# Optimization experiments

Measured on AMD Instinct MI355X. Metric: run time of the kernel, lower is better.

## Reference

```python
import jax, jax.numpy as jnp
import numpy as np

N_NODES = 50000
N_EDGES = 800000
NC = 16
FDIM = 13
FHID = 64


def setup_inputs() -> dict:
    key = jax.random.key(0)
    ks = jax.random.split(key, 10)
    inp = {
        "hx": jax.random.normal(ks[0], (N_NODES, NC), jnp.float32),
        "edgefeats": jax.random.normal(ks[1], (N_EDGES, FDIM), jnp.float32),
        "idxn": jax.random.randint(ks[2], (N_EDGES,), 0, N_NODES, jnp.int32),
        "edge_dst": jnp.sort(jax.random.randint(ks[3], (N_EDGES,), 0, N_NODES, jnp.int32)),
        "fnet_w1": jax.random.normal(ks[4], (FDIM, FHID), jnp.float32) * 0.3,
        "fnet_b1": jnp.zeros((FHID,), jnp.float32),
        "fnet_w2": jax.random.normal(ks[5], (FHID, NC * NC), jnp.float32) * 0.05,
        "fnet_b2": jnp.zeros((NC * NC,), jnp.float32),
        "w_ih": jax.random.normal(ks[6], (3 * NC, NC), jnp.float32) * 0.25,
        "w_hh": jax.random.normal(ks[7], (3 * NC, NC), jnp.float32) * 0.25,
        "b_ih": jnp.zeros((3 * NC,), jnp.float32),
        "b_hh": jnp.zeros((3 * NC,), jnp.float32),
    }
    return inp


def _gru_cell(x, h, w_ih, w_hh, b_ih, b_hh):
    gi = x @ w_ih.T + b_ih  # [N, 3*nc]
    gh = h @ w_hh.T + b_hh
    i_r, i_z, i_n = jnp.split(gi, 3, axis=1)
    h_r, h_z, h_n = jnp.split(gh, 3, axis=1)
    r = jax.nn.sigmoid(i_r + h_r)
    z = jax.nn.sigmoid(i_z + h_z)
    n = jnp.tanh(i_n + r * h_n)
    return (1.0 - z) * n + z * h


def reference(hx, edgefeats, idxn, edge_dst, fnet_w1, fnet_b1, fnet_w2, fnet_b2,
              w_ih, w_hh, b_ih, b_hh):
    n_nodes, nc = hx.shape
    # Filter-generating network: per-edge [nc, nc] weight matrices (shared over iterations).
    w_flat = jax.nn.relu(edgefeats @ fnet_w1 + fnet_b1) @ fnet_w2 + fnet_b2
    W = w_flat.reshape(-1, nc, nc)  # [E, nc, nc]
    # Degree normalization per destination node.
    deg = jax.ops.segment_sum(jnp.ones_like(edge_dst, dtype=hx.dtype), edge_dst,
                              num_segments=n_nodes)
    inv_deg = (1.0 / jnp.maximum(deg, 1.0))[:, None]  # [N, 1]

    def gconv(h):
        msgs = jnp.einsum('ec,ecd->ed', h[idxn], W)  # gather + per-edge matmul
        agg = jax.ops.segment_sum(msgs, edge_dst, num_segments=n_nodes)
        return agg * inv_deg

    def cell(inp, h):
        return _gru_cell(inp, h, w_ih, w_hh, b_ih, b_hh)

    hxs = [hx]
    h1 = cell(gconv(hx), hx); hxs.append(h1)
    h2 = cell(gconv(h1), h1); hxs.append(h2)
    h3 = cell(gconv(h2), h2)
    s1 = h1 + h3; hxs.append(s1)
    h4 = cell(gconv(s1), s1); hxs.append(h4)
    h5 = cell(gconv(h4), h4)
    s2 = h3 + h5; hxs.append(s2)
    h6 = cell(gconv(s2), s2); hxs.append(h6)
    h7 = cell(gconv(h6), h6)
    s3 = h5 + h7; hxs.append(s3)
    h8 = cell(gconv(s3), s3); hxs.append(h8)
    h9 = cell(gconv(h8), h8)
    s4 = h7 + h9; hxs.append(s4)
    h10 = cell(gconv(s4), s4); hxs.append(h10)
    return jnp.concatenate(hxs, axis=1)  # cat_all=True -> [N, 11*nc]
```

## Files before the change

### kernel.cpp

```cpp
#include <hip/hip_runtime.h>

#define NN 50000
#define NE 800000
#define OUTC 176

typedef unsigned int uint32;
typedef short bf16x8 __attribute__((ext_vector_type(8)));
typedef float f32x4 __attribute__((ext_vector_type(4)));

__device__ __forceinline__ uint32 f2bf_rne(float f) {
  union { float f; uint32 u; } v; v.f = f;
  uint32 u = v.u;
  return (u + 0x7FFFu + ((u >> 16) & 1u)) >> 16;
}
__device__ __forceinline__ uint32 packbf2(float a, float b) {
  return f2bf_rne(a) | (f2bf_rne(b) << 16);
}
__device__ __forceinline__ float blo(uint32 u) {
  union { uint32 x; float f; } t; t.x = u << 16; return t.f;
}
__device__ __forceinline__ float bhi(uint32 u) {
  union { uint32 x; float f; } t; t.x = u & 0xFFFF0000u; return t.f;
}
__device__ __forceinline__ float bf2f(unsigned short v) {
  union { uint32 x; float f; } t; t.x = ((uint32)v) << 16; return t.f;
}
__device__ __forceinline__ float sb2f(uint32 w, int b) {
  return (float)((int)(w << (24 - 8 * b)) >> 24);
}

__global__ __launch_bounds__(256) void deg_count_kernel(const int* __restrict__ edst,
                                                        float* __restrict__ deg) {
  int e = blockIdx.x * 256 + threadIdx.x;
  if (e < NE) atomicAdd(&deg[edst[e]], 1.0f);
}

__global__ __launch_bounds__(256) void deg_inv_kernel(float* __restrict__ deg) {
  int n = blockIdx.x * 256 + threadIdx.x;
  if (n < NN) deg[n] = 1.0f / fmaxf(deg[n], 1.0f);
}

__global__ __launch_bounds__(256) void copy_col0_kernel(const float* __restrict__ hx,
                                                        float* __restrict__ out) {
  int n = blockIdx.x * 256 + threadIdx.x;
  if (n >= NN) return;
  const float4* s = reinterpret_cast<const float4*>(hx + (size_t)n * 16);
  float4* d = reinterpret_cast<float4*>(out + (size_t)n * OUTC);
  d[0] = s[0]; d[1] = s[1]; d[2] = s[2]; d[3] = s[3];
}

__global__ __launch_bounds__(256) void repack_w2_kernel(const float* __restrict__ w2,
                                                        float* __restrict__ w2t) {
  int i = blockIdx.x * 256 + threadIdx.x;
  if (i >= 256 * 1024) return;
  int d = i >> 10, r = i & 1023, k = r >> 4, c = r & 15;
  w2t[i] = w2[k * 256 + c * 16 + d];
}

__global__ __launch_bounds__(256) void repack_w2f_kernel(const float* __restrict__ w2,
                                                         unsigned short* __restrict__ w2f) {
  int i = blockIdx.x * 256 + threadIdx.x;
  if (i >= 16384) return;
  int jj = i & 7;
  int l = (i >> 3) & 63;
  int nbm = i >> 9;
  int m = nbm & 1, nb = nbm >> 1;
  int k = m * 32 + (l >> 4) * 8 + jj;
  int j = nb * 16 + (l & 15);
  w2f[i] = (unsigned short)f2bf_rne(w2[k * 256 + j]);
}

__global__ __launch_bounds__(256) void fnet_mfma_i8_kernel(
    const float* __restrict__ ef, const float* __restrict__ w1, const float* __restrict__ b1,
    const unsigned short* __restrict__ w2f, const float* __restrict__ b2,
    unsigned char* __restrict__ W, unsigned short* __restrict__ S, int wo) {
  __shared__ float efs[832];
  __shared__ short w2s[16384];
  const int wave = threadIdx.x >> 6;
  const int l = threadIdx.x & 63;
  const int wid = wo + blockIdx.x * 4 + wave;
  const int d = l & 15, kg = l >> 4;

#pragma unroll
  for (int i = 0; i < 8; ++i)
    reinterpret_cast<uint4*>(w2s)[threadIdx.x + 256 * i] =
        reinterpret_cast<const uint4*>(w2f)[threadIdx.x + 256 * i];
  long long E0 = ((long long)wo + (long long)blockIdx.x * 4) * 16;
  if (threadIdx.x < 208) {
    reinterpret_cast<float4*>(efs)[threadIdx.x] =
        reinterpret_cast<const float4*>(ef + E0 * 13)[threadIdx.x];
  }
  __syncthreads();

  const int eloc = wave * 16 + d;
  float f[13];
#pragma unroll
  for (int i = 0; i < 13; ++i) f[i] = efs[eloc * 13 + i];
  float ua[8], ub[8];
#pragma unroll
  for (int j = 0; j < 8; ++j) { ua[j] = b1[kg * 8 + j]; ub[j] = b1[32 + kg * 8 + j]; }
#pragma unroll
  for (int i = 0; i < 13; ++i) {
    const float4* wa = reinterpret_cast<const float4*>(w1 + i * 64 + kg * 8);
    const float4* wb = reinterpret_cast<const float4*>(w1 + i * 64 + 32 + kg * 8);
    float4 a0 = wa[0], a1 = wa[1], c0 = wb[0], c1 = wb[1];
    float fi = f[i];
    ua[0] = fmaf(fi, a0.x, ua[0]); ua[1] = fmaf(fi, a0.y, ua[1]);
    ua[2] = fmaf(fi, a0.z, ua[2]); ua[3] = fmaf(fi, a0.w, ua[3]);
    ua[4] = fmaf(fi, a1.x, ua[4]); ua[5] = fmaf(fi, a1.y, ua[5]);
    ua[6] = fmaf(fi, a1.z, ua[6]); ua[7] = fmaf(fi, a1.w, ua[7]);
    ub[0] = fmaf(fi, c0.x, ub[0]); ub[1] = fmaf(fi, c0.y, ub[1]);
    ub[2] = fmaf(fi, c0.z, ub[2]); ub[3] = fmaf(fi, c0.w, ub[3]);
    ub[4] = fmaf(fi, c1.x, ub[4]); ub[5] = fmaf(fi, c1.y, ub[5]);
    ub[6] = fmaf(fi, c1.z, ub[6]); ub[7] = fmaf(fi, c1.w, ub[7]);
  }
  bf16x8 afrag0, afrag1;
#pragma unroll
  for (int j = 0; j < 8; ++j) {
    afrag0[j] = (short)f2bf_rne(fmaxf(ua[j], 0.0f));
    afrag1[j] = (short)f2bf_rne(fmaxf(ub[j], 0.0f));
  }

  float bias[16];
#pragma unroll
  for (int nb = 0; nb < 16; ++nb) bias[nb] = b2[nb * 16 + d];

  const bf16x8* Bp = reinterpret_cast<const bf16x8*>(w2s);
  f32x4 acc[16];
#pragma unroll
  for (int nb = 0; nb < 16; ++nb) {
    f32x4 c; c[0] = bias[nb]; c[1] = bias[nb]; c[2] = bias[nb]; c[3] = bias[nb];
    bf16x8 bf0 = Bp[(nb * 2 + 0) * 64 + l];
    bf16x8 bf1 = Bp[(nb * 2 + 1) * 64 + l];
    c = __builtin_amdgcn_mfma_f32_16x16x32_bf16(afrag0, bf0, c, 0, 0, 0);
    c = __builtin_amdgcn_mfma_f32_16x16x32_bf16(afrag1, bf1, c, 0, 0, 0);
    acc[nb] = c;
  }

  float mx[4];
#pragma unroll
  for (int r = 0; r < 4; ++r) {
    float m = 0.0f;
#pragma unroll
    for (int c = 0; c < 16; ++c) m = fmaxf(m, fabsf(acc[c][r]));
    mx[r] = m;
  }
#pragma unroll
  for (int mask = 1; mask < 16; mask <<= 1) {
#pragma unroll
    for (int r = 0; r < 4; ++r) mx[r] = fmaxf(mx[r], __shfl_xor(mx[r], mask));
  }
  uint32 sb[4]; float sinv[4];
#pragma unroll
  for (int r = 0; r < 4; ++r) {
    sb[r] = f2bf_rne(mx[r] * (1.0f / 127.0f));
    float sd = bf2f((unsigned short)sb[r]);
    sinv[r] = (sd > 0.0f) ? (1.0f / sd) : 0.0f;
  }
  if (d == 0) {
    uint32 lo = sb[0] | (sb[1] << 16), hi = sb[2] | (sb[3] << 16);
    *reinterpret_cast<uint2*>(S + (size_t)wid * 16 + kg * 4) = make_uint2(lo, hi);
  }

#pragma unroll
  for (int r = 0; r < 4; ++r) {
    size_t er = (size_t)wid * 16 + kg * 4 + r;
    uint32 p[4];
#pragma unroll
    for (int q = 0; q < 4; ++q) {
      uint32 wv = 0;
#pragma unroll
      for (int b = 0; b < 4; ++b) {
        float qf = fminf(127.0f, fmaxf(-127.0f, rintf(acc[q * 4 + b][r] * sinv[r])));
        wv |= ((uint32)((int)qf & 255)) << (8 * b);
      }
      p[q] = wv;
    }
    *reinterpret_cast<uint4*>(W + (er << 8) + (d << 4)) = make_uint4(p[0], p[1], p[2], p[3]);
  }
}

__device__ __forceinline__ void fnet_layer1(const float* __restrict__ ef, long long e,
                                            const float* __restrict__ w1,
                                            const float* __restrict__ b1,
                                            float* u) {
  float f[13];
#pragma unroll
  for (int i = 0; i < 13; ++i) f[i] = ef[(size_t)e * 13 + i];
#pragma unroll
  for (int k = 0; k < 64; ++k) u[k] = b1[k];
#pragma unroll
  for (int i = 0; i < 13; ++i) {
    float fi = f[i];
#pragma unroll
    for (int k = 0; k < 64; ++k) u[k] = fmaf(fi, w1[i * 64 + k], u[k]);
  }
#pragma unroll
  for (int k = 0; k < 64; ++k) u[k] = fmaxf(u[k], 0.0f);
}

__global__ __launch_bounds__(256) void fnet_bf16_kernel(
    const float* __restrict__ ef, const float* __restrict__ w1, const float* __restrict__ b1,
    const float* __restrict__ w2t, const float* __restrict__ b2,
    unsigned short* __restrict__ W, long long ebase, int ecnt) {
  int t = blockIdx.x * 256 + threadIdx.x;
  if (t >= ecnt) return;
  float u[64];
  fnet_layer1(ef, ebase + t, w1, b1, u);
#pragma unroll 1
  for (int dt = 0; dt < 8; ++dt) {
    uint32 p[16];
#pragma unroll
    for (int dd = 0; dd < 2; ++dd) {
      const int d = dt * 2 + dd;
      const float* wr = w2t + ((size_t)d << 10);
      float acc[16];
#pragma unroll
      for (int c = 0; c < 16; ++c) acc[c] = b2[c * 16 + d];
#pragma unroll
      for (int k = 0; k < 64; ++k) {
        float uk = u[k];
#pragma unroll
        for (int c = 0; c < 16; ++c) acc[c] = fmaf(uk, wr[k * 16 + c], acc[c]);
      }
#pragma unroll
      for (int q = 0; q < 8; ++q) p[dd * 8 + q] = packbf2(acc[2 * q], acc[2 * q + 1]);
    }
    uint4* dp = reinterpret_cast<uint4*>(W + ((size_t)t << 8) + (dt << 5));
    dp[0] = make_uint4(p[0], p[1], p[2], p[3]);
    dp[1] = make_uint4(p[4], p[5], p[6], p[7]);
    dp[2] = make_uint4(p[8], p[9], p[10], p[11]);
    dp[3] = make_uint4(p[12], p[13], p[14], p[15]);
  }
}

__global__ __launch_bounds__(256) void msg_bf16_kernel(
    const float* __restrict__ h, int h_ld,
    const unsigned short* __restrict__ W, long long ebase, int ecnt,
    const int* __restrict__ idxn, const int* __restrict__ edst,
    float* __restrict__ agg) {
  int t = blockIdx.x * 256 + threadIdx.x;
  if (t >= ecnt) return;
  int g = t >> 4, d = t & 15;
  int cur = -1;
  float acc = 0.0f;
  for (int s = 0; s < 16; ++s) {
    int erel = g * 16 + s;
    long long e = ebase + erel;
    int dst = edst[e];
    if (dst != cur) {
      if (cur >= 0) atomicAdd(&agg[(size_t)cur * 16 + d], acc);
      cur = dst; acc = 0.0f;
    }
    int src = idxn[e];
    const float4* hp = reinterpret_cast<const float4*>(h + (size_t)src * h_ld);
    float4 a0 = hp[0], a1 = hp[1], a2 = hp[2], a3 = hp[3];
    const uint4* wp = reinterpret_cast<const uint4*>(W + ((size_t)erel << 8) + (d << 4));
    uint4 w0 = wp[0], w1 = wp[1];
    acc = fmaf(a0.x, blo(w0.x), acc); acc = fmaf(a0.y, bhi(w0.x), acc);
    acc = fmaf(a0.z, blo(w0.y), acc); acc = fmaf(a0.w, bhi(w0.y), acc);
    acc = fmaf(a1.x, blo(w0.z), acc); acc = fmaf(a1.y, bhi(w0.z), acc);
    acc = fmaf(a1.z, blo(w0.w), acc); acc = fmaf(a1.w, bhi(w0.w), acc);
    acc = fmaf(a2.x, blo(w1.x), acc); acc = fmaf(a2.y, bhi(w1.x), acc);
    acc = fmaf(a2.z, blo(w1.y), acc); acc = fmaf(a2.w, bhi(w1.y), acc);
    acc = fmaf(a3.x, blo(w1.z), acc); acc = fmaf(a3.y, bhi(w1.z), acc);
    acc = fmaf(a3.z, blo(w1.w), acc); acc = fmaf(a3.w, bhi(w1.w), acc);
  }
  if (cur >= 0) atomicAdd(&agg[(size_t)cur * 16 + d], acc);
}

__device__ __forceinline__ float edge_dot_i8(const float4& a0, const float4& a1,
                                             const float4& a2, const float4& a3,
                                             const uint4& wv) {
  float r = 0.0f;
  r = fmaf(a0.x, sb2f(wv.x, 0), r); r = fmaf(a0.y, sb2f(wv.x, 1), r);
  r = fmaf(a0.z, sb2f(wv.x, 2), r); r = fmaf(a0.w, sb2f(wv.x, 3), r);
  r = fmaf(a1.x, sb2f(wv.y, 0), r); r = fmaf(a1.y, sb2f(wv.y, 1), r);
  r = fmaf(a1.z, sb2f(wv.y, 2), r); r = fmaf(a1.w, sb2f(wv.y, 3), r);
  r = fmaf(a2.x, sb2f(wv.z, 0), r); r = fmaf(a2.y, sb2f(wv.z, 1), r);
  r = fmaf(a2.z, sb2f(wv.z, 2), r); r = fmaf(a2.w, sb2f(wv.z, 3), r);
  r = fmaf(a3.x, sb2f(wv.w, 0), r); r = fmaf(a3.y, sb2f(wv.w, 1), r);
  r = fmaf(a3.z, sb2f(wv.w, 2), r); r = fmaf(a3.w, sb2f(wv.w, 3), r);
  return r;
}

__global__ __launch_bounds__(256) void msg_i8_kernel(
    const float* __restrict__ h, int h_ld,
    const unsigned char* __restrict__ W, const unsigned short* __restrict__ S,
    const int* __restrict__ idxn, const int* __restrict__ edst,
    float* __restrict__ agg) {
  int t = blockIdx.x * 256 + threadIdx.x;
  if (t >= NE / 2) return;
  const int g = t >> 4, d = t & 15;
  const int eA0 = g * 32;
  const int eB0 = g * 32 + 16;

  int curA = -1, curB = -1;
  float accA = 0.0f, accB = 0.0f;
#pragma unroll
  for (int s = 0; s < 16; ++s) {
    int eA = eA0 + s, eB = eB0 + s;
    int dstA = edst[eA], dstB = edst[eB];
    int srcA = idxn[eA], srcB = idxn[eB];
    const float4* hpA = reinterpret_cast<const float4*>(h + (size_t)srcA * h_ld);
    const float4* hpB = reinterpret_cast<const float4*>(h + (size_t)srcB * h_ld);
    float4 a0 = hpA[0], a1 = hpA[1], a2 = hpA[2], a3 = hpA[3];
    float4 b0 = hpB[0], b1 = hpB[1], b2 = hpB[2], b3 = hpB[3];
    uint4 wvA = *reinterpret_cast<const uint4*>(W + ((size_t)eA << 8) + (d << 4));
    uint4 wvB = *reinterpret_cast<const uint4*>(W + ((size_t)eB << 8) + (d << 4));
    float scA = bf2f(S[eA]), scB = bf2f(S[eB]);
    if (dstA != curA) {
      if (curA >= 0) atomicAdd(&agg[(size_t)curA * 16 + d], accA);
      curA = dstA; accA = 0.0f;
    }
    if (dstB != curB) {
      if (curB >= 0) atomicAdd(&agg[(size_t)curB * 16 + d], accB);
      curB = dstB; accB = 0.0f;
    }
    accA = fmaf(edge_dot_i8(a0, a1, a2, a3, wvA), scA, accA);
    accB = fmaf(edge_dot_i8(b0, b1, b2, b3, wvB), scB, accB);
  }
  atomicAdd(&agg[(size_t)curA * 16 + d], accA);
  atomicAdd(&agg[(size_t)curB * 16 + d], accB);
}

__global__ __launch_bounds__(256) void cell_kernel(
    const float* __restrict__ agg, const float* __restrict__ invd,
    const float* hin, int hin_ld,
    const float* __restrict__ wih, const float* __restrict__ whh,
    const float* __restrict__ bih, const float* __restrict__ bhh,
    float* hout, int hout_ld,
    const float* sprev, int sprev_ld,
    float* sout, int sout_ld,
    float* hdn) {
  int t = blockIdx.x * 256 + threadIdx.x;
  int n = t >> 4, j = t & 15;
  if (n >= NN) return;
  float inv = invd[n];
  float x[16], h[16];
  const float4* ap = reinterpret_cast<const float4*>(agg + (size_t)n * 16);
  const float4* hp = reinterpret_cast<const float4*>(hin + (size_t)n * hin_ld);
#pragma unroll
  for (int q = 0; q < 4; ++q) {
    float4 a = ap[q];
    x[4 * q + 0] = a.x * inv; x[4 * q + 1] = a.y * inv;
    x[4 * q + 2] = a.z * inv; x[4 * q + 3] = a.w * inv;
    float4 hv4 = hp[q];
    h[4 * q + 0] = hv4.x; h[4 * q + 1] = hv4.y;
    h[4 * q + 2] = hv4.z; h[4 * q + 3] = hv4.w;
  }
  const float4* wr4 = reinterpret_cast<const float4*>(wih + j * 16);
  const float4* wz4 = reinterpret_cast<const float4*>(wih + (16 + j) * 16);
  const float4* wn4 = reinterpret_cast<const float4*>(wih + (32 + j) * 16);
  const float4* vr4 = reinterpret_cast<const float4*>(whh + j * 16);
  const float4* vz4 = reinterpret_cast<const float4*>(whh + (16 + j) * 16);
  const float4* vn4 = reinterpret_cast<const float4*>(whh + (32 + j) * 16);
  float gr = bih[j], gz = bih[16 + j], gn = bih[32 + j];
  float hr = bhh[j], hz = bhh[16 + j], hn = bhh[32 + j];
#pragma unroll
  for (int q = 0; q < 4; ++q) {
    float4 wr = wr4[q], wz = wz4[q], wn = wn4[q];
    float4 vr = vr4[q], vz = vz4[q], vn = vn4[q];
    gr = fmaf(x[4 * q + 0], wr.x, gr); gr = fmaf(x[4 * q + 1], wr.y, gr);
    gr = fmaf(x[4 * q + 2], wr.z, gr); gr = fmaf(x[4 * q + 3], wr.w, gr);
    gz = fmaf(x[4 * q + 0], wz.x, gz); gz = fmaf(x[4 * q + 1], wz.y, gz);
    gz = fmaf(x[4 * q + 2], wz.z, gz); gz = fmaf(x[4 * q + 3], wz.w, gz);
    gn = fmaf(x[4 * q + 0], wn.x, gn); gn = fmaf(x[4 * q + 1], wn.y, gn);
    gn = fmaf(x[4 * q + 2], wn.z, gn); gn = fmaf(x[4 * q + 3], wn.w, gn);
    hr = fmaf(h[4 * q + 0], vr.x, hr); hr = fmaf(h[4 * q + 1], vr.y, hr);
    hr = fmaf(h[4 * q + 2], vr.z, hr); hr = fmaf(h[4 * q + 3], vr.w, hr);
    hz = fmaf(h[4 * q + 0], vz.x, hz); hz = fmaf(h[4 * q + 1], vz.y, hz);
    hz = fmaf(h[4 * q + 2], vz.z, hz); hz = fmaf(h[4 * q + 3], vz.w, hz);
    hn = fmaf(h[4 * q + 0], vn.x, hn); hn = fmaf(h[4 * q + 1], vn.y, hn);
    hn = fmaf(h[4 * q + 2], vn.z, hn); hn = fmaf(h[4 * q + 3], vn.w, hn);
  }
  float r = 1.0f / (1.0f + expf(-(gr + hr)));
  float z = 1.0f / (1.0f + expf(-(gz + hz)));
  float nng = tanhf(gn + r * hn);
  float hv = (1.0f - z) * nng + z * h[j];

  bool do_s = (sprev != nullptr);
  float sv = 0.0f;
  if (do_s) sv = hv + sprev[(size_t)n * sprev_ld + j];
  hout[(size_t)n * hout_ld + j] = hv;
  if (do_s) sout[(size_t)n * sout_ld + j] = sv;
  if (hdn != nullptr) hdn[(size_t)n * 16 + j] = do_s ? sv : hv;
}

extern "C" void kernel_launch(void* const* d_in, const int* in_sizes, int n_in,
                              void* d_out, int out_size, void* d_ws, size_t ws_size,
                              hipStream_t stream) {
  const float* hx   = (const float*)d_in[0];
  const float* ef   = (const float*)d_in[1];
  const int*   idxn = (const int*)d_in[2];
  const int*   edst = (const int*)d_in[3];
  const float* w1   = (const float*)d_in[4];
  const float* b1   = (const float*)d_in[5];
  const float* w2   = (const float*)d_in[6];
  const float* b2   = (const float*)d_in[7];
  const float* wih  = (const float*)d_in[8];
  const float* whh  = (const float*)d_in[9];
  const float* bih  = (const float*)d_in[10];
  const float* bhh  = (const float*)d_in[11];
  float* out = (float*)d_out;

  const size_t INV_OFF = 0;
  const size_t AGG_OFF = 200064;
  const size_t W2T_OFF = 3400192;
  const size_t HD_OFF  = W2T_OFF + 1048576;
  const size_t W_OFF   = HD_OFF + (size_t)NN * 64;
  if (ws_size < W_OFF + 1600 * 512) return;
  char* wsb = (char*)d_ws;
  float* invd = (float*)(wsb + INV_OFF);
  float* agg  = (float*)(wsb + AGG_OFF);
  float* w2t  = (float*)(wsb + W2T_OFF);
  unsigned short* w2f = (unsigned short*)(wsb + W2T_OFF);
  float* hd   = (float*)(wsb + HD_OFF);
  unsigned short* W16 = (unsigned short*)(wsb + W_OFF);
  unsigned char*  W8  = (unsigned char*)(wsb + W_OFF);
  unsigned short* S16 = (unsigned short*)(wsb + W_OFF + (size_t)NE * 256);
  size_t wrem = ws_size - W_OFF;

  int plan;
  size_t chunk = NE;
  if (wrem >= (size_t)NE * 260) plan = 1;
  else {
    plan = 2;
    chunk = (wrem / 512) & ~(size_t)15;
    if (chunk > NE) chunk = NE;
  }

  const int NB  = (NN + 255) / 256;
  const int EB  = (NE + 255) / 256;
  const int MB  = (NE / 2 + 255) / 256;
  const int CB  = (NN * 16 + 255) / 256;

  hipMemsetAsync(invd, 0, (size_t)NN * 4, stream);
  deg_count_kernel<<<EB, 256, 0, stream>>>(edst, invd);
  deg_inv_kernel<<<NB, 256, 0, stream>>>(invd);
  copy_col0_kernel<<<NB, 256, 0, stream>>>(hx, out);

  if (plan == 1) {
    repack_w2f_kernel<<<64, 256, 0, stream>>>(w2, w2f);
    for (int c = 0; c < 4; ++c)
      fnet_mfma_i8_kernel<<<3125, 256, 0, stream>>>(ef, w1, b1, w2f, b2, W8, S16,
                                                    c * 12500);
  } else {
    repack_w2_kernel<<<1024, 256, 0, stream>>>(w2, w2t);
  }

  auto col = [&](int c) { return out + (size_t)c * 16; };

  auto step = [&](const float* hin, int hin_ld, float* hout,
                  const float* sprev, float* sout, float* hdn) {
    hipMemsetAsync(agg, 0, (size_t)NN * 64, stream);
    if (plan == 1) {
      msg_i8_kernel<<<MB, 256, 0, stream>>>(hin, hin_ld, W8, S16, idxn, edst, agg);
    } else {
      for (size_t e0 = 0; e0 < NE; e0 += chunk) {
        int cnt = (int)(((size_t)NE - e0) < chunk ? ((size_t)NE - e0) : chunk);
        fnet_bf16_kernel<<<(cnt + 255) / 256, 256, 0, stream>>>(ef, w1, b1, w2t, b2, W16,
                                                                (long long)e0, cnt);
        msg_bf16_kernel<<<(cnt + 255) / 256, 256, 0, stream>>>(hin, hin_ld, W16,
                                                               (long long)e0, cnt,
                                                               idxn, edst, agg);
      }
    }
    cell_kernel<<<CB, 256, 0, stream>>>(agg, invd, hin, hin_ld, wih, whh, bih, bhh,
                                        hout, OUTC, sprev, OUTC, sout, OUTC, hdn);
  };

  step(hx, 16, col(1),  nullptr, nullptr, hd);
  step(hd, 16, col(2),  nullptr, nullptr, hd);
  step(hd, 16, col(10), col(1),  col(3),  hd);
  step(hd, 16, col(4),  nullptr, nullptr, hd);
  step(hd, 16, col(10), col(10), col(5),  hd);
  step(hd, 16, col(6),  nullptr, nullptr, hd);
  step(hd, 16, col(10), col(10), col(7),  hd);
  step(hd, 16, col(8),  nullptr, nullptr, hd);
  step(hd, 16, col(10), col(10), col(9),  hd);
  step(hd, 16, col(10), nullptr, nullptr, nullptr);
}
```

Baseline: 988.3 us.

## Gather bf16 hidden state in message kernel and zero agg inside cell kernel

Hidden state for the edge gather is stored as bf16, which halves the bytes read per gathered source row in the message kernel. W loads are marked nontemporal. The per-step agg memset is replaced by zeroing agg inside the cell kernel after it is read, and the four fnet launches are merged into one. The cell kernel now reads the fp32 hidden input from the output columns. This adds bf16 rounding error on the gathered activations, and the plan-2 fallback no longer gets an up-to-date bf16 buffer path.

```diff
diff --git a/kernel.cpp b/kernel.cpp
--- a/kernel.cpp
+++ b/kernel.cpp
@@ -7,6 +7,7 @@
 typedef unsigned int uint32;
 typedef short bf16x8 __attribute__((ext_vector_type(8)));
 typedef float f32x4 __attribute__((ext_vector_type(4)));
+typedef unsigned int uint32x4 __attribute__((ext_vector_type(4)));
 
 __device__ __forceinline__ uint32 f2bf_rne(float f) {
   union { float f; uint32 u; } v; v.f = f;
@@ -47,6 +48,12 @@
   const float4* s = reinterpret_cast<const float4*>(hx + (size_t)n * 16);
   float4* d = reinterpret_cast<float4*>(out + (size_t)n * OUTC);
   d[0] = s[0]; d[1] = s[1]; d[2] = s[2]; d[3] = s[3];
+}
+
+__global__ __launch_bounds__(256) void hx2hd_kernel(const float* __restrict__ hx,
+                                                    unsigned short* __restrict__ hdb) {
+  int t = blockIdx.x * 256 + threadIdx.x;
+  if (t < NN * 16) hdb[t] = (unsigned short)f2bf_rne(hx[t]);
 }
 
 __global__ __launch_bounds__(256) void repack_w2_kernel(const float* __restrict__ w2,
@@ -73,19 +80,19 @@
 __global__ __launch_bounds__(256) void fnet_mfma_i8_kernel(
     const float* __restrict__ ef, const float* __restrict__ w1, const float* __restrict__ b1,
     const unsigned short* __restrict__ w2f, const float* __restrict__ b2,
-    unsigned char* __restrict__ W, unsigned short* __restrict__ S, int wo) {
+    unsigned char* __restrict__ W, unsigned short* __restrict__ S) {
   __shared__ float efs[832];
   __shared__ short w2s[16384];
   const int wave = threadIdx.x >> 6;
   const int l = threadIdx.x & 63;
-  const int wid = wo + blockIdx.x * 4 + wave;
+  const int wid = blockIdx.x * 4 + wave;
   const int d = l & 15, kg = l >> 4;
 
 #pragma unroll
   for (int i = 0; i < 8; ++i)
     reinterpret_cast<uint4*>(w2s)[threadIdx.x + 256 * i] =
         reinterpret_cast<const uint4*>(w2f)[threadIdx.x + 256 * i];
-  long long E0 = ((long long)wo + (long long)blockIdx.x * 4) * 16;
+  long long E0 = (long long)blockIdx.x * 64;
   if (threadIdx.x < 208) {
     reinterpret_cast<float4*>(efs)[threadIdx.x] =
         reinterpret_cast<const float4*>(ef + E0 * 13)[threadIdx.x];
@@ -269,23 +276,22 @@
   if (cur >= 0) atomicAdd(&agg[(size_t)cur * 16 + d], acc);
 }
 
-__device__ __forceinline__ float edge_dot_i8(const float4& a0, const float4& a1,
-                                             const float4& a2, const float4& a3,
-                                             const uint4& wv) {
+__device__ __forceinline__ float edge_dot_i8bf(const uint32x4& h0, const uint32x4& h1,
+                                               const uint32x4& wv) {
   float r = 0.0f;
-  r = fmaf(a0.x, sb2f(wv.x, 0), r); r = fmaf(a0.y, sb2f(wv.x, 1), r);
-  r = fmaf(a0.z, sb2f(wv.x, 2), r); r = fmaf(a0.w, sb2f(wv.x, 3), r);
-  r = fmaf(a1.x, sb2f(wv.y, 0), r); r = fmaf(a1.y, sb2f(wv.y, 1), r);
-  r = fmaf(a1.z, sb2f(wv.y, 2), r); r = fmaf(a1.w, sb2f(wv.y, 3), r);
-  r = fmaf(a2.x, sb2f(wv.z, 0), r); r = fmaf(a2.y, sb2f(wv.z, 1), r);
-  r = fmaf(a2.z, sb2f(wv.z, 2), r); r = fmaf(a2.w, sb2f(wv.z, 3), r);
-  r = fmaf(a3.x, sb2f(wv.w, 0), r); r = fmaf(a3.y, sb2f(wv.w, 1), r);
-  r = fmaf(a3.z, sb2f(wv.w, 2), r); r = fmaf(a3.w, sb2f(wv.w, 3), r);
+  r = fmaf(blo(h0[0]), sb2f(wv[0], 0), r); r = fmaf(bhi(h0[0]), sb2f(wv[0], 1), r);
+  r = fmaf(blo(h0[1]), sb2f(wv[0], 2), r); r = fmaf(bhi(h0[1]), sb2f(wv[0], 3), r);
+  r = fmaf(blo(h0[2]), sb2f(wv[1], 0), r); r = fmaf(bhi(h0[2]), sb2f(wv[1], 1), r);
+  r = fmaf(blo(h0[3]), sb2f(wv[1], 2), r); r = fmaf(bhi(h0[3]), sb2f(wv[1], 3), r);
+  r = fmaf(blo(h1[0]), sb2f(wv[2], 0), r); r = fmaf(bhi(h1[0]), sb2f(wv[2], 1), r);
+  r = fmaf(blo(h1[1]), sb2f(wv[2], 2), r); r = fmaf(bhi(h1[1]), sb2f(wv[2], 3), r);
+  r = fmaf(blo(h1[2]), sb2f(wv[3], 0), r); r = fmaf(bhi(h1[2]), sb2f(wv[3], 1), r);
+  r = fmaf(blo(h1[3]), sb2f(wv[3], 2), r); r = fmaf(bhi(h1[3]), sb2f(wv[3], 3), r);
   return r;
 }
 
 __global__ __launch_bounds__(256) void msg_i8_kernel(
-    const float* __restrict__ h, int h_ld,
+    const unsigned short* __restrict__ hdb,
     const unsigned char* __restrict__ W, const unsigned short* __restrict__ S,
     const int* __restrict__ idxn, const int* __restrict__ edst,
     float* __restrict__ agg) {
@@ -302,12 +308,14 @@
     int eA = eA0 + s, eB = eB0 + s;
     int dstA = edst[eA], dstB = edst[eB];
     int srcA = idxn[eA], srcB = idxn[eB];
-    const float4* hpA = reinterpret_cast<const float4*>(h + (size_t)srcA * h_ld);
-    const float4* hpB = reinterpret_cast<const float4*>(h + (size_t)srcB * h_ld);
-    float4 a0 = hpA[0], a1 = hpA[1], a2 = hpA[2], a3 = hpA[3];
-    float4 b0 = hpB[0], b1 = hpB[1], b2 = hpB[2], b3 = hpB[3];
-    uint4 wvA = *reinterpret_cast<const uint4*>(W + ((size_t)eA << 8) + (d << 4));
-    uint4 wvB = *reinterpret_cast<const uint4*>(W + ((size_t)eB << 8) + (d << 4));
+    const uint32x4* hpA = reinterpret_cast<const uint32x4*>(hdb + (size_t)srcA * 16);
+    const uint32x4* hpB = reinterpret_cast<const uint32x4*>(hdb + (size_t)srcB * 16);
+    uint32x4 ha0 = hpA[0], ha1 = hpA[1];
+    uint32x4 hb0 = hpB[0], hb1 = hpB[1];
+    uint32x4 wvA = __builtin_nontemporal_load(
+        reinterpret_cast<const uint32x4*>(W + ((size_t)eA << 8) + (d << 4)));
+    uint32x4 wvB = __builtin_nontemporal_load(
+        reinterpret_cast<const uint32x4*>(W + ((size_t)eB << 8) + (d << 4)));
     float scA = bf2f(S[eA]), scB = bf2f(S[eB]);
     if (dstA != curA) {
       if (curA >= 0) atomicAdd(&agg[(size_t)curA * 16 + d], accA);
@@ -317,22 +325,22 @@
       if (curB >= 0) atomicAdd(&agg[(size_t)curB * 16 + d], accB);
       curB = dstB; accB = 0.0f;
     }
-    accA = fmaf(edge_dot_i8(a0, a1, a2, a3, wvA), scA, accA);
-    accB = fmaf(edge_dot_i8(b0, b1, b2, b3, wvB), scB, accB);
+    accA = fmaf(edge_dot_i8bf(ha0, ha1, wvA), scA, accA);
+    accB = fmaf(edge_dot_i8bf(hb0, hb1, wvB), scB, accB);
   }
   atomicAdd(&agg[(size_t)curA * 16 + d], accA);
   atomicAdd(&agg[(size_t)curB * 16 + d], accB);
 }
 
 __global__ __launch_bounds__(256) void cell_kernel(
-    const float* __restrict__ agg, const float* __restrict__ invd,
+    float* agg, const float* __restrict__ invd,
     const float* hin, int hin_ld,
     const float* __restrict__ wih, const float* __restrict__ whh,
     const float* __restrict__ bih, const float* __restrict__ bhh,
     float* hout, int hout_ld,
     const float* sprev, int sprev_ld,
     float* sout, int sout_ld,
-    float* hdn) {
+    unsigned short* hdn) {
   int t = blockIdx.x * 256 + threadIdx.x;
   int n = t >> 4, j = t & 15;
   if (n >= NN) return;
@@ -384,7 +392,10 @@
   if (do_s) sv = hv + sprev[(size_t)n * sprev_ld + j];
   hout[(size_t)n * hout_ld + j] = hv;
   if (do_s) sout[(size_t)n * sout_ld + j] = sv;
-  if (hdn != nullptr) hdn[(size_t)n * 16 + j] = do_s ? sv : hv;
+  if (hdn != nullptr) hdn[(size_t)n * 16 + j] = (unsigned short)f2bf_rne(do_s ? sv : hv);
+
+  asm volatile("" ::: "memory");
+  agg[(size_t)n * 16 + j] = 0.0f;
 }
 
 extern "C" void kernel_launch(void* const* d_in, const int* in_sizes, int n_in,
@@ -408,14 +419,14 @@
   const size_t AGG_OFF = 200064;
   const size_t W2T_OFF = 3400192;
   const size_t HD_OFF  = W2T_OFF + 1048576;
-  const size_t W_OFF   = HD_OFF + (size_t)NN * 64;
+  const size_t W_OFF   = HD_OFF + (size_t)NN * 32;
   if (ws_size < W_OFF + 1600 * 512) return;
   char* wsb = (char*)d_ws;
   float* invd = (float*)(wsb + INV_OFF);
   float* agg  = (float*)(wsb + AGG_OFF);
   float* w2t  = (float*)(wsb + W2T_OFF);
   unsigned short* w2f = (unsigned short*)(wsb + W2T_OFF);
-  float* hd   = (float*)(wsb + HD_OFF);
+  unsigned short* hdb = (unsigned short*)(wsb + HD_OFF);
   unsigned short* W16 = (unsigned short*)(wsb + W_OFF);
   unsigned char*  W8  = (unsigned char*)(wsb + W_OFF);
   unsigned short* S16 = (unsigned short*)(wsb + W_OFF + (size_t)NE * 256);
@@ -436,48 +447,48 @@
   const int CB  = (NN * 16 + 255) / 256;
 
   hipMemsetAsync(invd, 0, (size_t)NN * 4, stream);
+  hipMemsetAsync(agg, 0, (size_t)NN * 64, stream);
   deg_count_kernel<<<EB, 256, 0, stream>>>(edst, invd);
   deg_inv_kernel<<<NB, 256, 0, stream>>>(invd);
   copy_col0_kernel<<<NB, 256, 0, stream>>>(hx, out);
+  hx2hd_kernel<<<CB, 256, 0, stream>>>(hx, hdb);
 
   if (plan == 1) {
     repack_w2f_kernel<<<64, 256, 0, stream>>>(w2, w2f);
-    for (int c = 0; c < 4; ++c)
-      fnet_mfma_i8_kernel<<<3125, 256, 0, stream>>>(ef, w1, b1, w2f, b2, W8, S16,
-                                                    c * 12500);
+    fnet_mfma_i8_kernel<<<12500, 256, 0, stream>>>(ef, w1, b1, w2f, b2, W8, S16);
   } else {
     repack_w2_kernel<<<1024, 256, 0, stream>>>(w2, w2t);
   }
 
   auto col = [&](int c) { return out + (size_t)c * 16; };
 
-  auto step = [&](const float* hin, int hin_ld, float* hout,
-                  const float* sprev, float* sout, float* hdn) {
-    hipMemsetAsync(agg, 0, (size_t)NN * 64, stream);
+  auto step = [&](const float* hinF, int hin_ld, float* hout,
+                  const float* sprev, float* sout, unsigned short* hdn) {
     if (plan == 1) {
-      msg_i8_kernel<<<MB, 256, 0, stream>>>(hin, hin_ld, W8, S16, idxn, edst, agg);
+      msg_i8_kernel<<<MB, 256, 0, stream>>>(hdb, W8, S16, idxn, edst, agg);
     } else {
+      hipMemsetAsync(agg, 0, (size_t)NN * 64, stream);
       for (size_t e0 = 0; e0 < NE; e0 += chunk) {
         int cnt = (int)(((size_t)NE - e0) < chunk ? ((size_t)NE - e0) : chunk);
         fnet_bf16_kernel<<<(cnt + 255) / 256, 256, 0, stream>>>(ef, w1, b1, w2t, b2, W16,
                                                                 (long long)e0, cnt);
-        msg_bf16_kernel<<<(cnt + 255) / 256, 256, 0, stream>>>(hin, hin_ld, W16,
+        msg_bf16_kernel<<<(cnt + 255) / 256, 256, 0, stream>>>(hinF, hin_ld, W16,
                                                                (long long)e0, cnt,
                                                                idxn, edst, agg);
       }
     }
-    cell_kernel<<<CB, 256, 0, stream>>>(agg, invd, hin, hin_ld, wih, whh, bih, bhh,
+    cell_kernel<<<CB, 256, 0, stream>>>(agg, invd, hinF, hin_ld, wih, whh, bih, bhh,
                                         hout, OUTC, sprev, OUTC, sout, OUTC, hdn);
   };
 
-  step(hx, 16, col(1),  nullptr, nullptr, hd);
-  step(hd, 16, col(2),  nullptr, nullptr, hd);
-  step(hd, 16, col(10), col(1),  col(3),  hd);
-  step(hd, 16, col(4),  nullptr, nullptr, hd);
-  step(hd, 16, col(10), col(10), col(5),  hd);
-  step(hd, 16, col(6),  nullptr, nullptr, hd);
-  step(hd, 16, col(10), col(10), col(7),  hd);
-  step(hd, 16, col(8),  nullptr, nullptr, hd);
-  step(hd, 16, col(10), col(10), col(9),  hd);
-  step(hd, 16, col(10), nullptr, nullptr, nullptr);
-}
+  step(hx,      16,  col(1),  nullptr, nullptr, hdb);
+  step(col(1), OUTC, col(2),  nullptr, nullptr, hdb);
+  step(col(2), OUTC, col(10), col(1),  col(3),  hdb);
+  step(col(3), OUTC, col(4),  nullptr, nullptr, hdb);
+  step(col(4), OUTC, col(10), col(10), col(5),  hdb);
+  step(col(5), OUTC, col(6),  nullptr, nullptr, hdb);
+  step(col(6), OUTC, col(10), col(10), col(7),  hdb);
+  step(col(7), OUTC, col(8),  nullptr, nullptr, hdb);
+  step(col(8), OUTC, col(10), col(10), col(9),  hdb);
+  step(col(9), OUTC, col(10), nullptr, nullptr, nullptr);
+}
```

Result: faster. 963.8 us (-2.5%).
